# Kernel optimization log

Hardware: AMD Instinct MI355X
Metric: run time of the kernel (lower is better)

Reference implementation:

```python
import jax, jax.numpy as jnp
import numpy as np

N = 50000
E = 800000
IN = 128
HID = 32
HEADS = 4
OUT = 32
NEG_SLOPE = 0.2  # PyG GATConv default


def setup_inputs() -> dict:
    key = jax.random.key(0)
    ks = jax.random.split(key, 16)
    s = lambda k, sh: jax.random.normal(k, sh, jnp.float32) * 0.05
    inp = {}
    inp["x"] = jax.random.normal(ks[0], (N, IN), jnp.float32)
    inp["edge_idx"] = jax.random.randint(ks[1], (2, E), 0, N)
    inp["edge_attr"] = jax.random.normal(ks[2], (E, 1), jnp.float32)
    inp["lin1_w"] = s(ks[3], (IN, HEADS * HID))
    inp["att1_src"] = s(ks[4], (HEADS, HID))
    inp["att1_dst"] = s(ks[5], (HEADS, HID))
    inp["lin1_edge_w"] = s(ks[6], (1, HEADS * HID))
    inp["att1_edge"] = s(ks[7], (HEADS, HID))
    inp["bias1"] = jnp.zeros((HEADS * HID,), jnp.float32)
    inp["lin2_w"] = s(ks[8], (HEADS * HID, OUT))
    inp["att2_src"] = s(ks[9], (1, OUT))
    inp["att2_dst"] = s(ks[10], (1, OUT))
    inp["lin2_edge_w"] = s(ks[11], (1, OUT))
    inp["att2_edge"] = s(ks[12], (1, OUT))
    inp["bias2"] = jnp.zeros((OUT,), jnp.float32)
    return inp


def _gat_conv(x, src, dst, eattr, lin_w, a_src, a_dst, lin_e, a_e, bias, heads, ch, concat):
    """PyG GATConv (eval mode): gather -> leaky_relu logits -> segment softmax over dst -> scatter-sum."""
    n = x.shape[0]
    xl = (x @ lin_w).reshape(n, heads, ch)                      # [N,H,C]
    alpha = ((xl * a_src).sum(-1)[src]                          # [Etot,H]
             + (xl * a_dst).sum(-1)[dst]
             + ((eattr @ lin_e).reshape(-1, heads, ch) * a_e).sum(-1))
    alpha = jax.nn.leaky_relu(alpha, NEG_SLOPE)
    amax = jax.ops.segment_max(alpha, dst, num_segments=n)      # every node has a self-loop
    ex = jnp.exp(alpha - amax[dst])
    den = jax.ops.segment_sum(ex, dst, num_segments=n)
    w = ex / den[dst]                                           # [Etot,H]
    out = jax.ops.segment_sum(w[:, :, None] * xl[src], dst, num_segments=n)  # [N,H,C]
    out = out.reshape(n, heads * ch) if concat else out.mean(axis=1)
    return out + bias


def reference(x, edge_idx, edge_attr,
              lin1_w, att1_src, att1_dst, lin1_edge_w, att1_edge, bias1,
              lin2_w, att2_src, att2_dst, lin2_edge_w, att2_edge, bias2):
    n = x.shape[0]
    # add_self_loops=True with edge_attr fill_value='mean' (PyG default when edge_dim is set)
    loops = jnp.arange(n)
    src = jnp.concatenate([edge_idx[0], loops])
    dst = jnp.concatenate([edge_idx[1], loops])
    ea = jnp.concatenate(
        [edge_attr, jnp.broadcast_to(edge_attr.mean(0, keepdims=True), (n, edge_attr.shape[1]))], 0)
    h = jax.nn.elu(_gat_conv(x, src, dst, ea, lin1_w, att1_src, att1_dst,
                             lin1_edge_w, att1_edge, bias1, HEADS, HID, True))
    # F.dropout with training=False -> identity (eval mode)
    return _gat_conv(h, src, dst, ea, lin2_w, att2_src, att2_dst,
                     lin2_edge_w, att2_edge, bias2, 1, OUT, True)
```

## Files before the change

kernel.cpp:

```cpp
#include <hip/hip_runtime.h>
#include <hip/hip_fp16.h>
#include <math.h>

#define NN   50000
#define EE   800000
#define ETOT 850000
#define NEG  0.2f
#define SCAN_BLOCKS ((NN + 255) / 256)

#define O_DEG    0
#define O_EASUM  50000
#define ZERO_ELEMS 50004
#define O_COEF   50004
#define O_ROWPTR 50012
#define O_CURSOR 100016
#define O_BLKSUM 150016
#define O_SLOT   150528
#define O_ASRC1  1850528
#define O_ADST1  2050528
#define O_XLH    2250528
#define O_HLH    11850528
#define O_ASRC2  12650528
#define O_ADST2  12700528
#define WS_ELEMS 12750528

#define NODES_PER_GRP (NN / 8)

__global__ void k_ea_count(const float* __restrict__ ea, const int* __restrict__ ei,
                           const float* __restrict__ lew1, const float* __restrict__ ae1,
                           const float* __restrict__ lew2, const float* __restrict__ ae2,
                           float* __restrict__ easum, int* __restrict__ deg,
                           float* __restrict__ coef) {
  if (blockIdx.x == 0 && threadIdx.x < 128) {
    int t = threadIdx.x;
    float p = lew1[t] * ae1[t];
    #pragma unroll
    for (int o = 16; o > 0; o >>= 1) p += __shfl_down(p, o, 32);
    if ((t & 31) == 0) coef[t >> 5] = p;
    if (t < 32) {
      float q = lew2[t] * ae2[t];
      #pragma unroll
      for (int o = 16; o > 0; o >>= 1) q += __shfl_down(q, o, 32);
      if (t == 0) coef[4] = q;
    }
  }
  __shared__ float red[4];
  float s = 0.f;
  int stride = gridDim.x * blockDim.x;
  for (int i = blockIdx.x * blockDim.x + threadIdx.x; i < EE; i += stride) {
    s += ea[i];
    atomicAdd(deg + ei[EE + i], 1);
  }
  #pragma unroll
  for (int o = 32; o > 0; o >>= 1) s += __shfl_down(s, o, 64);
  if ((threadIdx.x & 63) == 0) red[threadIdx.x >> 6] = s;
  __syncthreads();
  if (threadIdx.x == 0) atomicAdd(easum, red[0] + red[1] + red[2] + red[3]);
}

__device__ __forceinline__ int wave_incl_scan(int v, int lane) {
  #pragma unroll
  for (int o = 1; o < 64; o <<= 1) {
    int u = __shfl_up(v, o, 64);
    if (lane >= o) v += u;
  }
  return v;
}

__global__ __launch_bounds__(256) void k_scan_blk(const int* __restrict__ deg,
                                                  int* __restrict__ rowptr,
                                                  int* __restrict__ blksum) {
  __shared__ int wsum[4];
  const int t = threadIdx.x;
  const int i = blockIdx.x * 256 + t;
  const int lane = t & 63, wv = t >> 6;
  int v = (i < NN) ? (deg[i] + 1) : 0;
  int incl = wave_incl_scan(v, lane);
  if (lane == 63) wsum[wv] = incl;
  __syncthreads();
  int off = 0;
  #pragma unroll
  for (int k = 0; k < 4; ++k) if (k < wv) off += wsum[k];
  incl += off;
  if (i < NN) rowptr[i] = incl - v;
  if (t == 255) blksum[blockIdx.x] = incl;
}

__global__ __launch_bounds__(256) void k_scan_add(int* __restrict__ rowptr,
                                                  int* __restrict__ cursor,
                                                  const int* __restrict__ blksum) {
  __shared__ int wsum[4];
  const int t = threadIdx.x;
  int v = (t < SCAN_BLOCKS && t < (int)blockIdx.x) ? blksum[t] : 0;
  #pragma unroll
  for (int o = 32; o > 0; o >>= 1) v += __shfl_down(v, o, 64);
  if ((t & 63) == 0) wsum[t >> 6] = v;
  __syncthreads();
  const int off = wsum[0] + wsum[1] + wsum[2] + wsum[3];
  const int i = blockIdx.x * 256 + t;
  if (i < NN) {
    int r = rowptr[i] + off;
    rowptr[i] = r;
    cursor[i] = r;
  }
  if (i == 0) rowptr[NN] = ETOT;
}

#define FILL_CHUNK  2048
#define FILL_NCHUNK ((ETOT + FILL_CHUNK - 1) / FILL_CHUNK)
__global__ __launch_bounds__(256) void k_fill(
    const int* __restrict__ ei, const float* __restrict__ eattr,
    const float* __restrict__ easum, int* __restrict__ cursor,
    unsigned* __restrict__ slot) {
  const int g    = blockIdx.x & 7;
  const int c    = blockIdx.x >> 3;
  const int dlo  = g * NODES_PER_GRP;
  const int dhi  = dlo + NODES_PER_GRP;
  const int base = c * FILL_CHUNK;
  #pragma unroll
  for (int it = 0; it < FILL_CHUNK / 256; ++it) {
    const int e = base + it * 256 + threadIdx.x;
    if (e < ETOT) {
      int d = (e < EE) ? ei[EE + e] : (e - EE);
      if (d >= dlo && d < dhi) {
        int s; float ea;
        if (e < EE) { s = ei[e]; ea = eattr[e]; }
        else { s = d; ea = easum[0] * (1.f / EE); }
        int sl = atomicAdd(cursor + d, 1);
        unsigned hb = (unsigned)__half_as_ushort(__float2half_rn(ea));
        slot[sl] = (unsigned)s | (hb << 16);
      }
    }
  }
}

#define GEMM_STEP(WB, K, XS) {                                              \
    const float4* Wr = (const float4*)((WB) + (size_t)(K));                 \
    _Pragma("unroll")                                                       \
    for (int j4 = 0; j4 < 8; ++j4) {                                        \
      float4 wv = Wr[j4];                                                   \
      acc[j4 * 4 + 0] += (XS) * wv.x;                                       \
      acc[j4 * 4 + 1] += (XS) * wv.y;                                       \
      acc[j4 * 4 + 2] += (XS) * wv.z;                                       \
      acc[j4 * 4 + 3] += (XS) * wv.w;                                       \
    } }

#define L1_NB ((NN + 63) / 64)
__global__ __launch_bounds__(256) void k_lin1(
    const float* __restrict__ x, const float* __restrict__ W,
    const float* __restrict__ att_src, const float* __restrict__ att_dst,
    __half* __restrict__ xlh, float* __restrict__ asrc, float* __restrict__ adst) {
  const int h   = __builtin_amdgcn_readfirstlane(threadIdx.x >> 6);
  const int n   = blockIdx.x * 64 + (threadIdx.x & 63);
  const int nc  = n < NN ? n : NN - 1;
  const float4* xr = (const float4*)(x + (size_t)nc * 128);
  const float*  Wh = W + h * 32;
  float acc[32];
  #pragma unroll
  for (int j = 0; j < 32; ++j) acc[j] = 0.f;
  float4 xv = xr[0];
  for (int kt = 0; kt < 32; ++kt) {
    float4 cur = xv;
    if (kt < 31) xv = xr[kt + 1];
    GEMM_STEP(Wh, (kt * 4 + 0) * 128, cur.x);
    GEMM_STEP(Wh, (kt * 4 + 1) * 128, cur.y);
    GEMM_STEP(Wh, (kt * 4 + 2) * 128, cur.z);
    GEMM_STEP(Wh, (kt * 4 + 3) * 128, cur.w);
  }
  if (n < NN) {
    __align__(16) __half hbuf[32];
    #pragma unroll
    for (int j = 0; j < 32; ++j) hbuf[j] = __float2half_rn(acc[j]);
    float4* dst = (float4*)(xlh + (size_t)n * 128 + h * 32);
    #pragma unroll
    for (int i = 0; i < 4; ++i) dst[i] = ((const float4*)hbuf)[i];
    float ss = 0.f, sd = 0.f;
    #pragma unroll
    for (int j = 0; j < 32; ++j) {
      ss += acc[j] * att_src[h * 32 + j];
      sd += acc[j] * att_dst[h * 32 + j];
    }
    asrc[n * 4 + h] = ss;
    adst[n * 4 + h] = sd;
  }
}

__global__ __launch_bounds__(256) void k_agg1l2(
    const int* __restrict__ rowptr, const unsigned* __restrict__ slot,
    const float* __restrict__ asrc, const float* __restrict__ adst,
    const float* __restrict__ coef, const __half* __restrict__ xlh,
    const float* __restrict__ bias1, const float* __restrict__ W2,
    const float* __restrict__ as2w, const float* __restrict__ ad2w,
    __half* __restrict__ hlh, float* __restrict__ asrc2, float* __restrict__ adst2) {
  __shared__ float rowbuf[8][132];
  int nl = threadIdx.x >> 5;
  int n = blockIdx.x * 8 + nl;
  if (n >= NN) return;
  int l = threadIdx.x & 31;
  int c4 = l << 2;
  int h = l >> 3;
  float cf = coef[h];
  float ad = adst[(size_t)n * 4 + h];
  int r0 = rowptr[n], r1 = rowptr[n + 1];
  float a0 = 0.f, a1 = 0.f, a2 = 0.f, a3 = 0.f, den = 0.f;
  for (int j = r0; j < r1; j += 4) {
    unsigned sd[4]; float asv[4]; uint2 raw[4];
    #pragma unroll
    for (int k = 0; k < 4; ++k) {
      int jj = (j + k < r1) ? (j + k) : (r1 - 1);
      sd[k] = slot[jj];
    }
    #pragma unroll
    for (int k = 0; k < 4; ++k) {
      int sn = (int)(sd[k] & 0xFFFFu);
      asv[k] = asrc[(size_t)sn * 4 + h];
      raw[k] = *(const uint2*)(xlh + (size_t)sn * 128 + c4);
    }
    #pragma unroll
    for (int k = 0; k < 4; ++k) {
      float eav = __half2float(__ushort_as_half((unsigned short)(sd[k] >> 16)));
      float alpha = asv[k] + ad + eav * cf;
      alpha = alpha > 0.f ? alpha : NEG * alpha;
      float ex = (j + k < r1) ? __expf(alpha) : 0.f;
      __half2 p0, p1;
      *(unsigned int*)&p0 = raw[k].x;
      *(unsigned int*)&p1 = raw[k].y;
      float2 f0 = __half22float2(p0), f1 = __half22float2(p1);
      a0 += ex * f0.x;
      a1 += ex * f0.y;
      a2 += ex * f1.x;
      a3 += ex * f1.y;
      den += ex;
    }
  }
  float inv = 1.f / den;
  float4 b = *(const float4*)(bias1 + c4);
  float v0 = a0 * inv + b.x, v1 = a1 * inv + b.y;
  float v2 = a2 * inv + b.z, v3 = a3 * inv + b.w;
  v0 = v0 > 0.f ? v0 : (expf(v0) - 1.f);
  v1 = v1 > 0.f ? v1 : (expf(v1) - 1.f);
  v2 = v2 > 0.f ? v2 : (expf(v2) - 1.f);
  v3 = v3 > 0.f ? v3 : (expf(v3) - 1.f);
  rowbuf[nl][c4 + 0] = v0;
  rowbuf[nl][c4 + 1] = v1;
  rowbuf[nl][c4 + 2] = v2;
  rowbuf[nl][c4 + 3] = v3;
  const int col = l;
  const float* rw = rowbuf[nl];
  float hsum = 0.f;
  #pragma unroll 4
  for (int k = 0; k < 128; ++k) hsum += rw[k] * W2[k * 32 + col];
  hlh[(size_t)n * 32 + col] = __float2half_rn(hsum);
  float ps = hsum * as2w[col];
  float pd = hsum * ad2w[col];
  #pragma unroll
  for (int o = 1; o < 32; o <<= 1) {
    ps += __shfl_xor(ps, o, 64);
    pd += __shfl_xor(pd, o, 64);
  }
  if (l == 0) {
    asrc2[n] = ps;
    adst2[n] = pd;
  }
}

__global__ __launch_bounds__(256) void k_agg2(
    const int* __restrict__ rowptr, const unsigned* __restrict__ slot,
    const float* __restrict__ asrc2, const float* __restrict__ adst2,
    const float* __restrict__ coef, const __half* __restrict__ hlh,
    const float* __restrict__ bias2, float* __restrict__ out) {
  int n = blockIdx.x * 32 + (threadIdx.x >> 3);
  if (n >= NN) return;
  int c4 = (threadIdx.x & 7) << 2;
  float cf = coef[4];
  float ad = adst2[n];
  int r0 = rowptr[n], r1 = rowptr[n + 1];
  float a0 = 0.f, a1 = 0.f, a2 = 0.f, a3 = 0.f, den = 0.f;
  for (int j = r0; j < r1; j += 4) {
    unsigned sd[4]; float asv[4]; uint2 raw[4];
    #pragma unroll
    for (int k = 0; k < 4; ++k) {
      int jj = (j + k < r1) ? (j + k) : (r1 - 1);
      sd[k] = slot[jj];
    }
    #pragma unroll
    for (int k = 0; k < 4; ++k) {
      int sn = (int)(sd[k] & 0xFFFFu);
      asv[k] = asrc2[sn];
      raw[k] = *(const uint2*)(hlh + (size_t)sn * 32 + c4);
    }
    #pragma unroll
    for (int k = 0; k < 4; ++k) {
      float eav = __half2float(__ushort_as_half((unsigned short)(sd[k] >> 16)));
      float alpha = asv[k] + ad + eav * cf;
      alpha = alpha > 0.f ? alpha : NEG * alpha;
      float ex = (j + k < r1) ? __expf(alpha) : 0.f;
      __half2 p0, p1;
      *(unsigned int*)&p0 = raw[k].x;
      *(unsigned int*)&p1 = raw[k].y;
      float2 f0 = __half22float2(p0), f1 = __half22float2(p1);
      a0 += ex * f0.x;
      a1 += ex * f0.y;
      a2 += ex * f1.x;
      a3 += ex * f1.y;
      den += ex;
    }
  }
  float inv = 1.f / den;
  float4 b = *(const float4*)(bias2 + c4);
  *(float4*)(out + (size_t)n * 32 + c4) =
      make_float4(a0 * inv + b.x, a1 * inv + b.y, a2 * inv + b.z, a3 * inv + b.w);
}

extern "C" void kernel_launch(void* const* d_in, const int* in_sizes, int n_in,
                              void* d_out, int out_size, void* d_ws, size_t ws_size,
                              hipStream_t stream) {
  const float* x        = (const float*)d_in[0];
  const int*   ei       = (const int*)d_in[1];
  const float* eattr    = (const float*)d_in[2];
  const float* lin1_w   = (const float*)d_in[3];
  const float* att1_src = (const float*)d_in[4];
  const float* att1_dst = (const float*)d_in[5];
  const float* lin1_ew  = (const float*)d_in[6];
  const float* att1_e   = (const float*)d_in[7];
  const float* bias1    = (const float*)d_in[8];
  const float* lin2_w   = (const float*)d_in[9];
  const float* att2_src = (const float*)d_in[10];
  const float* att2_dst = (const float*)d_in[11];
  const float* lin2_ew  = (const float*)d_in[12];
  const float* att2_e   = (const float*)d_in[13];
  const float* bias2    = (const float*)d_in[14];
  float* out = (float*)d_out;
  float* ws  = (float*)d_ws;
  int*   wsi = (int*)d_ws;

  int*      deg     = wsi + O_DEG;
  float*    easum   = ws + O_EASUM;
  float*    coef    = ws + O_COEF;
  int*      rowptr  = wsi + O_ROWPTR;
  int*      cursor  = wsi + O_CURSOR;
  int*      blksum  = wsi + O_BLKSUM;
  unsigned* slot    = (unsigned*)(ws + O_SLOT);
  float*    asrc1   = ws + O_ASRC1;
  float*    adst1   = ws + O_ADST1;
  __half*   xlh     = (__half*)(ws + O_XLH);
  __half*   hlh     = (__half*)(ws + O_HLH);
  float*    asrc2   = ws + O_ASRC2;
  float*    adst2   = ws + O_ADST2;

  hipMemsetAsync(ws, 0, (size_t)ZERO_ELEMS * sizeof(float), stream);

  k_ea_count<<<256, 256, 0, stream>>>(eattr, ei, lin1_ew, att1_e, lin2_ew, att2_e,
                                      easum, deg, coef);

  k_scan_blk<<<SCAN_BLOCKS, 256, 0, stream>>>(deg, rowptr, blksum);
  k_scan_add<<<SCAN_BLOCKS, 256, 0, stream>>>(rowptr, cursor, blksum);
  k_fill<<<FILL_NCHUNK * 8, 256, 0, stream>>>(ei, eattr, easum, cursor, slot);

  k_lin1<<<L1_NB, 256, 0, stream>>>(x, lin1_w, att1_src, att1_dst, xlh, asrc1, adst1);

  k_agg1l2<<<(NN + 7) / 8, 256, 0, stream>>>(rowptr, slot, asrc1, adst1, coef, xlh,
                                             bias1, lin2_w, att2_src, att2_dst,
                                             hlh, asrc2, adst2);

  k_agg2<<<(NN + 31) / 32, 256, 0, stream>>>(rowptr, slot, asrc2, adst2, coef, hlh, bias2, out);
}
```

Baseline: 283.4 us.

## Store layer-1 features head-major and aggregate one head at a time

The projected features and attention scalars move from a node-major [N,4,32] layout to head-major [4,N,32] and [4,N]. The first-layer aggregation now loops over the four heads, with each lane gathering one half per edge from a 64-byte row instead of 8 bytes from a 256-byte row. The goal is a smaller per-head gather working set with better cache locality. In exchange the CSR slot list is read four times, the loop runs four times as long, and each gathered load is narrower.

```diff
diff --git a/kernel.cpp b/kernel.cpp
--- a/kernel.cpp
+++ b/kernel.cpp
@@ -171,7 +171,7 @@
     __align__(16) __half hbuf[32];
     #pragma unroll
     for (int j = 0; j < 32; ++j) hbuf[j] = __float2half_rn(acc[j]);
-    float4* dst = (float4*)(xlh + (size_t)n * 128 + h * 32);
+    float4* dst = (float4*)(xlh + (size_t)h * NN * 32 + (size_t)n * 32);
     #pragma unroll
     for (int i = 0; i < 4; ++i) dst[i] = ((const float4*)hbuf)[i];
     float ss = 0.f, sd = 0.f;
@@ -180,8 +180,8 @@
       ss += acc[j] * att_src[h * 32 + j];
       sd += acc[j] * att_dst[h * 32 + j];
     }
-    asrc[n * 4 + h] = ss;
-    adst[n * 4 + h] = sd;
+    asrc[(size_t)h * NN + n] = ss;
+    adst[(size_t)h * NN + n] = sd;
   }
 }
 
@@ -197,54 +197,41 @@
   int n = blockIdx.x * 8 + nl;
   if (n >= NN) return;
   int l = threadIdx.x & 31;
-  int c4 = l << 2;
-  int h = l >> 3;
-  float cf = coef[h];
-  float ad = adst[(size_t)n * 4 + h];
   int r0 = rowptr[n], r1 = rowptr[n + 1];
-  float a0 = 0.f, a1 = 0.f, a2 = 0.f, a3 = 0.f, den = 0.f;
-  for (int j = r0; j < r1; j += 4) {
-    unsigned sd[4]; float asv[4]; uint2 raw[4];
-    #pragma unroll
-    for (int k = 0; k < 4; ++k) {
-      int jj = (j + k < r1) ? (j + k) : (r1 - 1);
-      sd[k] = slot[jj];
-    }
-    #pragma unroll
-    for (int k = 0; k < 4; ++k) {
-      int sn = (int)(sd[k] & 0xFFFFu);
-      asv[k] = asrc[(size_t)sn * 4 + h];
-      raw[k] = *(const uint2*)(xlh + (size_t)sn * 128 + c4);
-    }
-    #pragma unroll
-    for (int k = 0; k < 4; ++k) {
-      float eav = __half2float(__ushort_as_half((unsigned short)(sd[k] >> 16)));
-      float alpha = asv[k] + ad + eav * cf;
-      alpha = alpha > 0.f ? alpha : NEG * alpha;
-      float ex = (j + k < r1) ? __expf(alpha) : 0.f;
-      __half2 p0, p1;
-      *(unsigned int*)&p0 = raw[k].x;
-      *(unsigned int*)&p1 = raw[k].y;
-      float2 f0 = __half22float2(p0), f1 = __half22float2(p1);
-      a0 += ex * f0.x;
-      a1 += ex * f0.y;
-      a2 += ex * f1.x;
-      a3 += ex * f1.y;
-      den += ex;
-    }
-  }
-  float inv = 1.f / den;
-  float4 b = *(const float4*)(bias1 + c4);
-  float v0 = a0 * inv + b.x, v1 = a1 * inv + b.y;
-  float v2 = a2 * inv + b.z, v3 = a3 * inv + b.w;
-  v0 = v0 > 0.f ? v0 : (expf(v0) - 1.f);
-  v1 = v1 > 0.f ? v1 : (expf(v1) - 1.f);
-  v2 = v2 > 0.f ? v2 : (expf(v2) - 1.f);
-  v3 = v3 > 0.f ? v3 : (expf(v3) - 1.f);
-  rowbuf[nl][c4 + 0] = v0;
-  rowbuf[nl][c4 + 1] = v1;
-  rowbuf[nl][c4 + 2] = v2;
-  rowbuf[nl][c4 + 3] = v3;
+  #pragma unroll 1
+  for (int h = 0; h < 4; ++h) {
+    float cf = coef[h];
+    float ad = adst[(size_t)h * NN + n];
+    const float*  ash = asrc + (size_t)h * NN;
+    const __half* xh  = xlh + (size_t)h * NN * 32;
+    float a = 0.f, den = 0.f;
+    for (int j = r0; j < r1; j += 4) {
+      unsigned sd[4]; float asv[4]; __half xv[4];
+      #pragma unroll
+      for (int k = 0; k < 4; ++k) {
+        int jj = (j + k < r1) ? (j + k) : (r1 - 1);
+        sd[k] = slot[jj];
+      }
+      #pragma unroll
+      for (int k = 0; k < 4; ++k) {
+        int sn = (int)(sd[k] & 0xFFFFu);
+        asv[k] = ash[sn];
+        xv[k]  = xh[(size_t)sn * 32 + l];
+      }
+      #pragma unroll
+      for (int k = 0; k < 4; ++k) {
+        float eav = __half2float(__ushort_as_half((unsigned short)(sd[k] >> 16)));
+        float alpha = asv[k] + ad + eav * cf;
+        alpha = alpha > 0.f ? alpha : NEG * alpha;
+        float ex = (j + k < r1) ? __expf(alpha) : 0.f;
+        a += ex * __half2float(xv[k]);
+        den += ex;
+      }
+    }
+    float v = a / den + bias1[h * 32 + l];
+    v = v > 0.f ? v : (expf(v) - 1.f);
+    rowbuf[nl][h * 32 + l] = v;
+  }
   const int col = l;
   const float* rw = rowbuf[nl];
   float hsum = 0.f;
```

Measured after the change: 340.5 us. 20.1% more time.
